# Kernel optimization log

Measured on AMD Instinct MI355X. Metric: run time of the kernel, lower is better.

The kernel has to match this reference:

```python
import jax, jax.numpy as jnp
import numpy as np

N = 4096
NEG_SLOPE = 0.2


def _gat_layer(x, src, dst, W, Wb, a, ab):
    # h = Linear(x); e_ij = a([h_i, h_j]) for each edge; dense softmax over dim=1; ELU
    h = x @ W + Wb                               # [N, D]
    D = h.shape[-1]
    e = h[src] @ a[:D] + h[dst] @ a[D:] + ab     # [E] per-edge attention logits
    n = x.shape[0]
    attn = jnp.full((n, n), -jnp.inf, dtype=x.dtype).at[src, dst].set(e)
    attn = jnp.where(attn > 0, attn, NEG_SLOPE * attn)   # leaky_relu (keeps -inf)
    attn = jax.nn.softmax(attn, axis=1)
    return jax.nn.elu(attn @ h)                  # sigma = ELU


def _multihead(x, src, dst, hW, hWb, ha, hab, oW, oWb, oa, oab):
    # concat=False: mean over head outputs, then out GATLayer
    heads = jax.vmap(lambda W, Wb, a, ab: _gat_layer(x, src, dst, W, Wb, a, ab))(hW, hWb, ha, hab)
    xm = heads.mean(axis=0)
    return _gat_layer(xm, src, dst, oW, oWb, oa, oab)


def setup_inputs() -> dict:
    key = jax.random.key(0)
    ks = jax.random.split(key, 20)
    in_dim, hid, out_dim, H, E = 512, 256, 128, 4, 131072
    x = jax.random.normal(ks[0], (N, in_dim), jnp.float32)
    edge_index = jax.random.randint(ks[1], (2, E), 0, N)
    # force self loops so every softmax row has at least one finite entry
    edge_index = edge_index.at[:, :N].set(jnp.broadcast_to(jnp.arange(N), (2, N)))

    def lin(k, shape, fan_in):
        return jax.random.uniform(k, shape, jnp.float32, -1.0, 1.0) / np.sqrt(fan_in).astype(np.float32)

    return {
        "x": x,
        "edge_index": edge_index,
        # layer 0 (MultiHeadGAT in_dim->hid)
        "l0_hW": lin(ks[2], (H, in_dim, hid), in_dim),
        "l0_hWb": lin(ks[3], (H, hid), in_dim),
        "l0_ha": lin(ks[4], (H, 2 * hid), 2 * hid),
        "l0_hab": lin(ks[5], (H,), 2 * hid),
        "l0_oW": lin(ks[6], (hid, hid), hid),
        "l0_oWb": lin(ks[7], (hid,), hid),
        "l0_oa": lin(ks[8], (2 * hid,), 2 * hid),
        "l0_oab": lin(ks[9], (), 2 * hid),
        # layer 1 (MultiHeadGAT hid->hid)
        "l1_hW": lin(ks[10], (H, hid, hid), hid),
        "l1_hWb": lin(ks[11], (H, hid), hid),
        "l1_ha": lin(ks[12], (H, 2 * hid), 2 * hid),
        "l1_hab": lin(ks[13], (H,), 2 * hid),
        "l1_oW": lin(ks[14], (hid, hid), hid),
        "l1_oWb": lin(ks[15], (hid,), hid),
        "l1_oa": lin(ks[16], (2 * hid,), 2 * hid),
        "l1_oab": lin(ks[17], (), 2 * hid),
        # final Linear(hid -> out_dim)
        "lin_W": lin(ks[18], (hid, out_dim), hid),
        "lin_b": lin(ks[19], (out_dim,), hid),
    }


def reference(x, edge_index, l0_hW, l0_hWb, l0_ha, l0_hab, l0_oW, l0_oWb, l0_oa, l0_oab,
              l1_hW, l1_hWb, l1_ha, l1_hab, l1_oW, l1_oWb, l1_oa, l1_oab, lin_W, lin_b):
    src, dst = edge_index[0], edge_index[1]
    lrelu = lambda v: jnp.where(v > 0, v, NEG_SLOPE * v)
    h = lrelu(_multihead(x, src, dst, l0_hW, l0_hWb, l0_ha, l0_hab, l0_oW, l0_oWb, l0_oa, l0_oab))
    h = lrelu(_multihead(h, src, dst, l1_hW, l1_hWb, l1_ha, l1_hab, l1_oW, l1_oWb, l1_oa, l1_oab))
    return h @ lin_W + lin_b  # [N, out_dim], flatten(1) is a no-op for 2D
```

## Files before the change

### kernel.cpp

```cpp
#include <hip/hip_runtime.h>
#include <hip/hip_bf16.h>
#include <math.h>

#define NEG_SLOPE 0.2f

constexpr int D = 256;
constexpr int HEADS = 4;
constexpr int MAXDEG = 2048;

typedef __attribute__((ext_vector_type(8))) short short8;
typedef __attribute__((ext_vector_type(4))) float floatx4;

__device__ inline unsigned short bf16_hi_trunc(float v) {
  return (unsigned short)(__float_as_uint(v) >> 16);
}
__device__ inline float bf16_tof(unsigned short u) {
  return __uint_as_float(((unsigned int)u) << 16);
}
__device__ inline unsigned short bf16_rn(float v) {
  unsigned int b = __float_as_uint(v);
  b += 0x7fffu + ((b >> 16) & 1u);
  return (unsigned short)(b >> 16);
}
__device__ inline void split2(float v, unsigned short& hi, unsigned short& lo) {
  hi = bf16_hi_trunc(v);
  lo = bf16_rn(v - bf16_tof(hi));
}

__global__ void zero_ints(int* __restrict__ p, int n) {
  int i = blockIdx.x * blockDim.x + threadIdx.x;
  if (i < n) p[i] = 0;
}

__global__ void count_kernel(const int* __restrict__ src, int* __restrict__ cnt, int E) {
  int k = blockIdx.x * blockDim.x + threadIdx.x;
  if (k < E) atomicAdd(&cnt[src[k]], 1);
}

__global__ __launch_bounds__(256) void scan_kernel(const int* __restrict__ cnt,
                                                   int* __restrict__ row_ptr, int Nn) {
  __shared__ int part[256];
  int tid = threadIdx.x;
  int per = Nn >> 8;
  int base = tid * per;
  int local[32];
  int s = 0;
  for (int j = 0; j < per; ++j) { local[j] = cnt[base + j]; s += local[j]; }
  part[tid] = s;
  __syncthreads();
  for (int off = 1; off < 256; off <<= 1) {
    int v = (tid >= off) ? part[tid - off] : 0;
    __syncthreads();
    part[tid] += v;
    __syncthreads();
  }
  int run = part[tid] - s;
  for (int j = 0; j < per; ++j) { row_ptr[base + j] = run; run += local[j]; }
  if (tid == 255) row_ptr[Nn] = run;
}

__global__ void fill_kernel(const int* __restrict__ src, const int* __restrict__ dst,
                            const int* __restrict__ row_ptr, int* __restrict__ cursor,
                            int* __restrict__ col, int E) {
  int k = blockIdx.x * blockDim.x + threadIdx.x;
  if (k < E) {
    int s = src[k];
    int pos = atomicAdd(&cursor[s], 1);
    col[row_ptr[s] + pos] = dst[k];
  }
}

__global__ __launch_bounds__(256) void dedupe_kernel(const int* __restrict__ row_ptr,
                                                     int* __restrict__ col, int Nn) {
  __shared__ int cs[MAXDEG];
  int i = blockIdx.x;
  int start = row_ptr[i];
  int len = row_ptr[i + 1] - start;
  if (len > MAXDEG) len = MAXDEG;
  int tid = threadIdx.x;
  for (int t = tid; t < len; t += 256) cs[t] = col[start + t];
  __syncthreads();
  for (int t = tid; t < len; t += 256) {
    int c = cs[t];
    bool dup = false;
    for (int s2 = 0; s2 < t; ++s2)
      if (cs[s2] == c) { dup = true; break; }
    if (dup) col[start + t] = -1;
  }
}

__global__ void split_kernel(const float* __restrict__ in, unsigned short* __restrict__ hi,
                             unsigned short* __restrict__ lo, int n4) {
  int idx = blockIdx.x * blockDim.x + threadIdx.x;
  if (idx < n4) {
    float4 v = ((const float4*)in)[idx];
    ushort4 h, l;
    split2(v.x, h.x, l.x);
    split2(v.y, h.y, l.y);
    split2(v.z, h.z, l.z);
    split2(v.w, h.w, l.w);
    ((ushort4*)hi)[idx] = h;
    ((ushort4*)lo)[idx] = l;
  }
}

__global__ __launch_bounds__(256) void transpose_split_kernel(
    const float* __restrict__ B, unsigned short* __restrict__ Thi,
    unsigned short* __restrict__ Tlo, int K, int N) {
  __shared__ float tile[32][33];
  const int t = threadIdx.x;
  const int k0 = blockIdx.x * 32, n0 = blockIdx.y * 32, h = blockIdx.z;
  const float* Bh = B + (size_t)h * K * N;
  const int tr = t >> 5, tc = t & 31;
#pragma unroll
  for (int i = 0; i < 4; ++i)
    tile[tr + 8 * i][tc] = Bh[(size_t)(k0 + tr + 8 * i) * N + (n0 + tc)];
  __syncthreads();
  unsigned short* ThiH = Thi + (size_t)h * N * K;
  unsigned short* TloH = Tlo + (size_t)h * N * K;
#pragma unroll
  for (int i = 0; i < 4; ++i) {
    int n = n0 + tr + 8 * i, k = k0 + tc;
    float v = tile[tc][tr + 8 * i];
    unsigned short hi, lo;
    split2(v, hi, lo);
    ThiH[(size_t)n * K + k] = hi;
    TloH[(size_t)n * K + k] = lo;
  }
}

__global__ __launch_bounds__(256) void transpose_split7_kernel(
    const float* __restrict__ l1hW, const float* __restrict__ B0,
    const float* __restrict__ B1, const float* __restrict__ B2,
    unsigned short* __restrict__ l1Thi, unsigned short* __restrict__ l1Tlo,
    unsigned short* __restrict__ T0h, unsigned short* __restrict__ T0l,
    unsigned short* __restrict__ T1h, unsigned short* __restrict__ T1l,
    unsigned short* __restrict__ T2h, unsigned short* __restrict__ T2l) {
  const int z = blockIdx.z;
  const int N = (z == 6) ? 128 : 256;
  const int K = 256;
  const int k0 = blockIdx.x * 32, n0 = blockIdx.y * 32;
  if (n0 >= N) return;
  const float* B;
  unsigned short *Thi, *Tlo;
  if (z < 4) {
    B = l1hW + (size_t)z * K * 256;
    Thi = l1Thi + (size_t)z * 256 * K;
    Tlo = l1Tlo + (size_t)z * 256 * K;
  } else if (z == 4) { B = B0; Thi = T0h; Tlo = T0l; }
  else if (z == 5)   { B = B1; Thi = T1h; Tlo = T1l; }
  else               { B = B2; Thi = T2h; Tlo = T2l; }
  __shared__ float tile[32][33];
  const int t = threadIdx.x;
  const int tr = t >> 5, tc = t & 31;
#pragma unroll
  for (int i = 0; i < 4; ++i)
    tile[tr + 8 * i][tc] = B[(size_t)(k0 + tr + 8 * i) * N + (n0 + tc)];
  __syncthreads();
#pragma unroll
  for (int i = 0; i < 4; ++i) {
    int n = n0 + tr + 8 * i, k = k0 + tc;
    float v = tile[tc][tr + 8 * i];
    unsigned short hi, lo;
    split2(v, hi, lo);
    Thi[(size_t)n * K + k] = hi;
    Tlo[(size_t)n * K + k] = lo;
  }
}

__global__ __launch_bounds__(256) void gemm_mfma_split(
    const unsigned short* __restrict__ Ahi, const unsigned short* __restrict__ Alo,
    const unsigned short* __restrict__ Bthi, const unsigned short* __restrict__ Btlo,
    const float* __restrict__ bias, float* __restrict__ C, unsigned short* __restrict__ Cb,
    const float* __restrict__ aptr, float* __restrict__ alphaB, float* __restrict__ betaB,
    int M, int N, int K) {
  constexpr int LSTR = 72;
  __shared__ unsigned short sA[2][64 * LSTR];
  __shared__ unsigned short sB[2][64 * LSTR];
  const int tid = threadIdx.x;
  const int bm = blockIdx.x * 64;
  const int gn = blockIdx.y * 64;
  const int head = (gn) / N;
  const int bn = gn - head * N;

  const int lane = tid & 63;
  const int wv = tid >> 6;
  const int wm = (wv & 1) * 32;
  const int wn = (wv >> 1) * 32;
  const int q = lane >> 4;
  const int l15 = lane & 15;

  floatx4 acc[2][2];
#pragma unroll
  for (int i = 0; i < 2; ++i)
#pragma unroll
    for (int j = 0; j < 2; ++j) acc[i][j] = (floatx4)0.0f;

  for (int k0 = 0; k0 < K; k0 += 64) {
    short8 ra[2][2], rb[2][2];
#pragma unroll
    for (int i = 0; i < 2; ++i) {
      const int c = tid + 256 * i;
      const int row = c >> 3, koff = (c & 7) << 3;
      const size_t aoff = (size_t)(bm + row) * K + k0 + koff;
      const size_t boff = (size_t)(gn + row) * K + k0 + koff;
      ra[0][i] = *(const short8*)(Ahi + aoff);
      ra[1][i] = *(const short8*)(Alo + aoff);
      rb[0][i] = *(const short8*)(Bthi + boff);
      rb[1][i] = *(const short8*)(Btlo + boff);
    }
    __syncthreads();
#pragma unroll
    for (int i = 0; i < 2; ++i) {
      const int c = tid + 256 * i;
      const int row = c >> 3, koff = (c & 7) << 3;
      *(short8*)(&sA[0][row * LSTR + koff]) = ra[0][i];
      *(short8*)(&sA[1][row * LSTR + koff]) = ra[1][i];
      *(short8*)(&sB[0][row * LSTR + koff]) = rb[0][i];
      *(short8*)(&sB[1][row * LSTR + koff]) = rb[1][i];
    }
    __syncthreads();
#pragma unroll
    for (int kc = 0; kc < 2; ++kc) {
      const int ko = kc * 32 + q * 8;
      short8 aH[2], aL[2], bH[2], bL[2];
#pragma unroll
      for (int i = 0; i < 2; ++i) {
        aH[i] = *(const short8*)(&sA[0][(wm + i * 16 + l15) * LSTR + ko]);
        aL[i] = *(const short8*)(&sA[1][(wm + i * 16 + l15) * LSTR + ko]);
        bH[i] = *(const short8*)(&sB[0][(wn + i * 16 + l15) * LSTR + ko]);
        bL[i] = *(const short8*)(&sB[1][(wn + i * 16 + l15) * LSTR + ko]);
      }
#pragma unroll
      for (int i = 0; i < 2; ++i)
#pragma unroll
        for (int j = 0; j < 2; ++j) {
          acc[i][j] = __builtin_amdgcn_mfma_f32_16x16x32_bf16(aH[i], bH[j], acc[i][j], 0, 0, 0);
          acc[i][j] = __builtin_amdgcn_mfma_f32_16x16x32_bf16(aH[i], bL[j], acc[i][j], 0, 0, 0);
          acc[i][j] = __builtin_amdgcn_mfma_f32_16x16x32_bf16(aL[i], bH[j], acc[i][j], 0, 0, 0);
        }
    }
  }
  const size_t cBase = (size_t)head * M * N;
  const int colh0 = bn + wn + l15;
  const int colh1 = colh0 + 16;
  const float bv0 = bias[head * N + colh0];
  const float bv1 = bias[head * N + colh1];
  float as0 = 0.f, as1 = 0.f, ad0 = 0.f, ad1 = 0.f;
  if (aptr) {
    as0 = aptr[head * 2 * N + colh0];
    as1 = aptr[head * 2 * N + colh1];
    ad0 = aptr[head * 2 * N + N + colh0];
    ad1 = aptr[head * 2 * N + N + colh1];
  }
#pragma unroll
  for (int i = 0; i < 2; ++i) {
    const int rowb = bm + wm + i * 16 + q * 4;
#pragma unroll
    for (int r = 0; r < 4; ++r) {
      const float o0 = acc[i][0][r] + bv0;
      const float o1 = acc[i][1][r] + bv1;
      if (Cb) {
        Cb[cBase + (size_t)(rowb + r) * N + colh0] = bf16_rn(o0);
        Cb[cBase + (size_t)(rowb + r) * N + colh1] = bf16_rn(o1);
      } else {
        C[cBase + (size_t)(rowb + r) * N + colh0] = o0;
        C[cBase + (size_t)(rowb + r) * N + colh1] = o1;
      }
      if (aptr) {
        float pa = o0 * as0 + o1 * as1;
        float pb = o0 * ad0 + o1 * ad1;
#pragma unroll
        for (int off = 1; off < 16; off <<= 1) {
          pa += __shfl_xor(pa, off, 64);
          pb += __shfl_xor(pb, off, 64);
        }
        if (l15 == 0) {
          atomicAdd(&alphaB[head * M + rowb + r], pa);
          atomicAdd(&betaB[head * M + rowb + r], pb);
        }
      }
    }
  }
}

__global__ __launch_bounds__(256) void gemm_bias(
    const float* __restrict__ A, const float* __restrict__ B,
    const float* __restrict__ bias, float* __restrict__ C,
    int M, int N, int K) {
  __shared__ float As[16][68];
  __shared__ float Bs[16][68];
  const int tid = threadIdx.x;
  const int bm = blockIdx.x * 64;
  const int gn = blockIdx.y * 64;
  const int head = gn / N;
  const int bn = gn - head * N;
  const float* Bh = B + (size_t)head * K * N;

  const int tx = tid & 15;
  const int ty = tid >> 4;
  const int am = tid >> 2;
  const int ak = (tid & 3) << 2;
  const int bk = tid >> 4;
  const int bn4 = (tid & 15) << 2;

  float acc[4][4] = {};

  for (int k0 = 0; k0 < K; k0 += 16) {
    float4 av = *(const float4*)(A + (size_t)(bm + am) * K + (k0 + ak));
    float4 bv = *(const float4*)(Bh + (size_t)(k0 + bk) * N + (bn + bn4));
    __syncthreads();
    As[ak + 0][am] = av.x;
    As[ak + 1][am] = av.y;
    As[ak + 2][am] = av.z;
    As[ak + 3][am] = av.w;
    *(float4*)(&Bs[bk][bn4]) = bv;
    __syncthreads();
#pragma unroll
    for (int k = 0; k < 16; ++k) {
      float4 aa = *(const float4*)(&As[k][ty << 2]);
      float4 bb = *(const float4*)(&Bs[k][tx << 2]);
      acc[0][0] += aa.x * bb.x; acc[0][1] += aa.x * bb.y; acc[0][2] += aa.x * bb.z; acc[0][3] += aa.x * bb.w;
      acc[1][0] += aa.y * bb.x; acc[1][1] += aa.y * bb.y; acc[1][2] += aa.y * bb.z; acc[1][3] += aa.y * bb.w;
      acc[2][0] += aa.z * bb.x; acc[2][1] += aa.z * bb.y; acc[2][2] += aa.z * bb.z; acc[2][3] += aa.z * bb.w;
      acc[3][0] += aa.w * bb.x; acc[3][1] += aa.w * bb.y; acc[3][2] += aa.w * bb.z; acc[3][3] += aa.w * bb.w;
    }
  }
  float* Ch = C + (size_t)head * M * N;
  const float* bh = bias + (size_t)head * N;
  const int ccol = bn + (tx << 2);
  float4 bias4 = *(const float4*)(bh + ccol);
#pragma unroll
  for (int r = 0; r < 4; ++r) {
    int row = bm + (ty << 2) + r;
    float4 o;
    o.x = acc[r][0] + bias4.x;
    o.y = acc[r][1] + bias4.y;
    o.z = acc[r][2] + bias4.z;
    o.w = acc[r][3] + bias4.w;
    *(float4*)(Ch + (size_t)row * N + ccol) = o;
  }
}

__global__ __launch_bounds__(256) void alphabeta_kernel(
    const float* __restrict__ h, const float* __restrict__ a,
    float* __restrict__ alpha, float* __restrict__ beta, int Nn) {
  __shared__ float reda[4], redb[4];
  const int i = blockIdx.x;
  const int hh = blockIdx.y;
  const int tid = threadIdx.x;
  const int lane = tid & 63, wid = tid >> 6;
  float v = h[((size_t)hh * Nn + i) * D + tid];
  float pa = v * a[hh * 2 * D + tid];
  float pb = v * a[hh * 2 * D + D + tid];
#pragma unroll
  for (int off = 32; off > 0; off >>= 1) {
    pa += __shfl_xor(pa, off, 64);
    pb += __shfl_xor(pb, off, 64);
  }
  if (lane == 0) { reda[wid] = pa; redb[wid] = pb; }
  __syncthreads();
  if (tid == 0) {
    alpha[hh * Nn + i] = reda[0] + reda[1] + reda[2] + reda[3];
    beta[hh * Nn + i] = redb[0] + redb[1] + redb[2] + redb[3];
  }
}

template <int BF16H>
__global__ __launch_bounds__(256) void attn2(
    const float* __restrict__ h, const unsigned short* __restrict__ hB,
    const float* __restrict__ alpha, const float* __restrict__ beta,
    const float* __restrict__ ab, const int* __restrict__ row_ptr,
    const int* __restrict__ col, float* __restrict__ out,
    unsigned short* __restrict__ oHi, unsigned short* __restrict__ oLo,
    int Nn, int H, int mode) {
  const int tid = threadIdx.x;
  const int lane = tid & 63;
  const int wv = tid >> 6;
  const int bx = blockIdx.x;
  const int head = bx % H;
  const int rowblk = bx / H;
  const int i = rowblk * 4 + wv;

  const float* hL = BF16H ? nullptr : (h + (size_t)head * Nn * D + (lane << 2));
  const unsigned short* hLB = BF16H ? (hB + (size_t)head * Nn * D + (lane << 2)) : nullptr;
  const float* betaH = beta + (size_t)head * Nn;
  const float ai = alpha[head * Nn + i] + ab[head];
  const int start = row_ptr[i];
  const int len = row_ptr[i + 1] - start;

  float m = -3.0e38f, s = 0.0f;
  float4 acc0 = make_float4(0.0f, 0.0f, 0.0f, 0.0f);
  float4 acc1 = make_float4(0.0f, 0.0f, 0.0f, 0.0f);

  for (int t0 = 0; t0 < len; t0 += 64) {
    const int t = t0 + lane;
    const int c = (t < len) ? col[start + t] : -1;
    float e = -3.0e38f;
    if (c >= 0) {
      e = ai + betaH[c];
      e = e > 0.0f ? e : NEG_SLOPE * e;
    }
    float cm = e;
#pragma unroll
    for (int off = 32; off > 0; off >>= 1) cm = fmaxf(cm, __shfl_xor(cm, off, 64));
    const float newm = fmaxf(m, cm);
    const float scale = __expf(m - newm);
    const float w = (c >= 0) ? __expf(e - newm) : 0.0f;
    float cs = w;
#pragma unroll
    for (int off = 32; off > 0; off >>= 1) cs += __shfl_xor(cs, off, 64);
    s = s * scale + cs;
    acc0.x *= scale; acc0.y *= scale; acc0.z *= scale; acc0.w *= scale;
    acc1.x *= scale; acc1.y *= scale; acc1.z *= scale; acc1.w *= scale;
    m = newm;

    const int cS = (c >= 0) ? c : 0;
    const int cnt = min(64, len - t0);
    int j = 0;
    if constexpr (BF16H) {
      for (; j + 4 <= cnt; j += 4) {
        const int c0 = __shfl(cS, j);     const float w0 = __shfl(w, j);
        const int c1 = __shfl(cS, j + 1); const float w1 = __shfl(w, j + 1);
        const int c2 = __shfl(cS, j + 2); const float w2 = __shfl(w, j + 2);
        const int c3 = __shfl(cS, j + 3); const float w3 = __shfl(w, j + 3);
        const ushort4 u0 = *(const ushort4*)(hLB + (size_t)c0 * D);
        const ushort4 u1 = *(const ushort4*)(hLB + (size_t)c1 * D);
        const ushort4 u2 = *(const ushort4*)(hLB + (size_t)c2 * D);
        const ushort4 u3 = *(const ushort4*)(hLB + (size_t)c3 * D);
        acc0.x += w0 * bf16_tof(u0.x); acc0.y += w0 * bf16_tof(u0.y);
        acc0.z += w0 * bf16_tof(u0.z); acc0.w += w0 * bf16_tof(u0.w);
        acc1.x += w1 * bf16_tof(u1.x); acc1.y += w1 * bf16_tof(u1.y);
        acc1.z += w1 * bf16_tof(u1.z); acc1.w += w1 * bf16_tof(u1.w);
        acc0.x += w2 * bf16_tof(u2.x); acc0.y += w2 * bf16_tof(u2.y);
        acc0.z += w2 * bf16_tof(u2.z); acc0.w += w2 * bf16_tof(u2.w);
        acc1.x += w3 * bf16_tof(u3.x); acc1.y += w3 * bf16_tof(u3.y);
        acc1.z += w3 * bf16_tof(u3.z); acc1.w += w3 * bf16_tof(u3.w);
      }
      for (; j < cnt; ++j) {
        const int cj = __shfl(cS, j);
        const float wj = __shfl(w, j);
        const ushort4 u = *(const ushort4*)(hLB + (size_t)cj * D);
        acc0.x += wj * bf16_tof(u.x); acc0.y += wj * bf16_tof(u.y);
        acc0.z += wj * bf16_tof(u.z); acc0.w += wj * bf16_tof(u.w);
      }
    } else {
      for (; j + 4 <= cnt; j += 4) {
        const int c0 = __shfl(cS, j);     const float w0 = __shfl(w, j);
        const int c1 = __shfl(cS, j + 1); const float w1 = __shfl(w, j + 1);
        const int c2 = __shfl(cS, j + 2); const float w2 = __shfl(w, j + 2);
        const int c3 = __shfl(cS, j + 3); const float w3 = __shfl(w, j + 3);
        const float4 h0 = *(const float4*)(hL + (size_t)c0 * D);
        const float4 h1 = *(const float4*)(hL + (size_t)c1 * D);
        const float4 h2 = *(const float4*)(hL + (size_t)c2 * D);
        const float4 h3 = *(const float4*)(hL + (size_t)c3 * D);
        acc0.x += w0 * h0.x; acc0.y += w0 * h0.y; acc0.z += w0 * h0.z; acc0.w += w0 * h0.w;
        acc1.x += w1 * h1.x; acc1.y += w1 * h1.y; acc1.z += w1 * h1.z; acc1.w += w1 * h1.w;
        acc0.x += w2 * h2.x; acc0.y += w2 * h2.y; acc0.z += w2 * h2.z; acc0.w += w2 * h2.w;
        acc1.x += w3 * h3.x; acc1.y += w3 * h3.y; acc1.z += w3 * h3.z; acc1.w += w3 * h3.w;
      }
      for (; j < cnt; ++j) {
        const int cj = __shfl(cS, j);
        const float wj = __shfl(w, j);
        const float4 hv = *(const float4*)(hL + (size_t)cj * D);
        acc0.x += wj * hv.x; acc0.y += wj * hv.y;
        acc0.z += wj * hv.z; acc0.w += wj * hv.w;
      }
    }
  }

  const float inv = 1.0f / s;
  float4 v;
  v.x = (acc0.x + acc1.x) * inv; v.y = (acc0.y + acc1.y) * inv;
  v.z = (acc0.z + acc1.z) * inv; v.w = (acc0.w + acc1.w) * inv;
  v.x = v.x > 0.0f ? v.x : expm1f(v.x);
  v.y = v.y > 0.0f ? v.y : expm1f(v.y);
  v.z = v.z > 0.0f ? v.z : expm1f(v.z);
  v.w = v.w > 0.0f ? v.w : expm1f(v.w);

  if (mode == 1 || mode == 3) {
    v.x = v.x > 0.0f ? v.x : NEG_SLOPE * v.x;
    v.y = v.y > 0.0f ? v.y : NEG_SLOPE * v.y;
    v.z = v.z > 0.0f ? v.z : NEG_SLOPE * v.z;
    v.w = v.w > 0.0f ? v.w : NEG_SLOPE * v.w;
    if (mode == 1) {
      *(float4*)(out + (size_t)i * D + (lane << 2)) = v;
    } else {
      ushort4 h4, l4;
      split2(v.x, h4.x, l4.x);
      split2(v.y, h4.y, l4.y);
      split2(v.z, h4.z, l4.z);
      split2(v.w, h4.w, l4.w);
      const size_t q4 = ((size_t)i * D >> 2) + lane;
      ((ushort4*)oHi)[q4] = h4;
      ((ushort4*)oLo)[q4] = l4;
    }
  } else if (mode == 0) {
    *(float4*)(out + ((size_t)head * Nn + i) * D + (lane << 2)) = v;
  } else {
    const float invH = 1.0f / (float)H;
    float* o = out + (size_t)i * D + (lane << 2);
    atomicAdd(o + 0, invH * v.x);
    atomicAdd(o + 1, invH * v.y);
    atomicAdd(o + 2, invH * v.z);
    atomicAdd(o + 3, invH * v.w);
  }
}

__global__ __launch_bounds__(256) void mean4_kernel(
    float* __restrict__ hsep, unsigned short* __restrict__ outHi,
    unsigned short* __restrict__ outLo, int total4, int mode) {
  int idx = blockIdx.x * blockDim.x + threadIdx.x;
  if (idx < total4) {
    float4* p = (float4*)hsep;
    float4 a = p[idx], b = p[idx + total4], c = p[idx + 2 * total4], d = p[idx + 3 * total4];
    float4 o;
    o.x = 0.25f * (a.x + b.x + c.x + d.x);
    o.y = 0.25f * (a.y + b.y + c.y + d.y);
    o.z = 0.25f * (a.z + b.z + c.z + d.z);
    o.w = 0.25f * (a.w + b.w + c.w + d.w);
    if (mode == 0) {
      p[idx] = o;
    } else {
      ushort4 h4, l4;
      split2(o.x, h4.x, l4.x);
      split2(o.y, h4.y, l4.y);
      split2(o.z, h4.z, l4.z);
      split2(o.w, h4.w, l4.w);
      ((ushort4*)outHi)[idx] = h4;
      ((ushort4*)outLo)[idx] = l4;
    }
  }
}

__global__ void zero_floats(float* __restrict__ p, int n) {
  int i = blockIdx.x * blockDim.x + threadIdx.x;
  if (i < n) p[i] = 0.0f;
}

extern "C" void kernel_launch(void* const* d_in, const int* in_sizes, int n_in,
                              void* d_out, int out_size, void* d_ws, size_t ws_size,
                              hipStream_t stream) {
  const float* x = (const float*)d_in[0];
  const int* eidx = (const int*)d_in[1];
  const float* l0_hW = (const float*)d_in[2];
  const float* l0_hWb = (const float*)d_in[3];
  const float* l0_ha = (const float*)d_in[4];
  const float* l0_hab = (const float*)d_in[5];
  const float* l0_oW = (const float*)d_in[6];
  const float* l0_oWb = (const float*)d_in[7];
  const float* l0_oa = (const float*)d_in[8];
  const float* l0_oab = (const float*)d_in[9];
  const float* l1_hW = (const float*)d_in[10];
  const float* l1_hWb = (const float*)d_in[11];
  const float* l1_ha = (const float*)d_in[12];
  const float* l1_hab = (const float*)d_in[13];
  const float* l1_oW = (const float*)d_in[14];
  const float* l1_oWb = (const float*)d_in[15];
  const float* l1_oa = (const float*)d_in[16];
  const float* l1_oab = (const float*)d_in[17];
  const float* lin_W = (const float*)d_in[18];
  const float* lin_b = (const float*)d_in[19];

  const int in_dim = 512;
  const int Nn = in_sizes[0] / in_dim;
  const int E = in_sizes[1] / 2;
  const int out_dim = 128;

  char* wsp = (char*)d_ws;
  auto alloc = [&](size_t bytes) {
    char* p = wsp;
    wsp += (bytes + 255) & ~(size_t)255;
    return p;
  };
  const size_t ndBytes = sizeof(float) * (size_t)Nn * D;
  const size_t mfmaNeed = 52000000;
  const bool mfma = ws_size >= mfmaNeed;

  if (mfma) {
    unsigned short* hbufB = (unsigned short*)alloc((size_t)HEADS * Nn * D * 2);
    unsigned short* houtB = (unsigned short*)alloc((size_t)Nn * D * 2);
    float* hsep   = (float*)alloc(ndBytes * HEADS);
    unsigned short* xhi  = (unsigned short*)alloc((size_t)Nn * in_dim * 2);
    unsigned short* xlo  = (unsigned short*)alloc((size_t)Nn * in_dim * 2);
    unsigned short* x1hi = xhi;
    unsigned short* x1lo = xlo;
    unsigned short* xmhi = (unsigned short*)alloc((size_t)Nn * D * 2);
    unsigned short* xmlo = (unsigned short*)alloc((size_t)Nn * D * 2);
    unsigned short* l0hHi = (unsigned short*)alloc((size_t)HEADS * in_dim * D * 2);
    unsigned short* l0hLo = (unsigned short*)alloc((size_t)HEADS * in_dim * D * 2);
    unsigned short* l1hHi = (unsigned short*)alloc((size_t)HEADS * D * D * 2);
    unsigned short* l1hLo = (unsigned short*)alloc((size_t)HEADS * D * D * 2);
    unsigned short* l0oHi = (unsigned short*)alloc((size_t)D * D * 2);
    unsigned short* l0oLo = (unsigned short*)alloc((size_t)D * D * 2);
    unsigned short* l1oHi = (unsigned short*)alloc((size_t)D * D * 2);
    unsigned short* l1oLo = (unsigned short*)alloc((size_t)D * D * 2);
    unsigned short* linHi = (unsigned short*)alloc((size_t)D * out_dim * 2);
    unsigned short* linLo = (unsigned short*)alloc((size_t)D * out_dim * 2);
    int* cnt     = (int*)alloc(sizeof(int) * Nn);
    int* cursor  = (int*)alloc(sizeof(int) * Nn);
    float* abz   = (float*)alloc(sizeof(float) * 4 * 2 * HEADS * (size_t)Nn);
    int* row_ptr = (int*)alloc(sizeof(int) * (Nn + 1));
    int* col     = (int*)alloc(sizeof(int) * E);
    auto alphaS = [&](int s) { return abz + (size_t)s * 2 * HEADS * Nn; };
    auto betaS  = [&](int s) { return abz + (size_t)s * 2 * HEADS * Nn + HEADS * Nn; };

    const int* src = eidx;
    const int* dst = eidx + E;

    const int zeroN = 2 * Nn + 4 * 2 * HEADS * Nn;
    zero_ints<<<(zeroN + 255) / 256, 256, 0, stream>>>(cnt, zeroN);
    count_kernel<<<(E + 255) / 256, 256, 0, stream>>>(src, cnt, E);
    scan_kernel<<<1, 256, 0, stream>>>(cnt, row_ptr, Nn);
    fill_kernel<<<(E + 255) / 256, 256, 0, stream>>>(src, dst, row_ptr, cursor, col, E);
    dedupe_kernel<<<Nn, 256, 0, stream>>>(row_ptr, col, Nn);

    split_kernel<<<(Nn * in_dim / 4 + 255) / 256, 256, 0, stream>>>(x, xhi, xlo, Nn * in_dim / 4);
    transpose_split_kernel<<<dim3(in_dim / 32, D / 32, HEADS), 256, 0, stream>>>(l0_hW, l0hHi, l0hLo, in_dim, D);
    transpose_split7_kernel<<<dim3(8, 8, 7), 256, 0, stream>>>(
        l1_hW, l0_oW, l1_oW, lin_W, l1hHi, l1hLo, l0oHi, l0oLo, l1oHi, l1oLo, linHi, linLo);

    const int total4 = Nn * D / 4;
    const int meanBlocks = (total4 + 255) / 256;

    gemm_mfma_split<<<dim3(Nn / 64, HEADS * D / 64), 256, 0, stream>>>(
        xhi, xlo, l0hHi, l0hLo, l0_hWb, nullptr, hbufB, l0_ha, alphaS(0), betaS(0), Nn, D, in_dim);
    attn2<1><<<HEADS * (Nn / 4), 256, 0, stream>>>(nullptr, hbufB, alphaS(0), betaS(0), l0_hab,
                                                   row_ptr, col, hsep, nullptr, nullptr, Nn, HEADS, 0);
    mean4_kernel<<<meanBlocks, 256, 0, stream>>>(hsep, xmhi, xmlo, total4, 1);
    gemm_mfma_split<<<dim3(Nn / 64, D / 64), 256, 0, stream>>>(
        xmhi, xmlo, l0oHi, l0oLo, l0_oWb, nullptr, houtB, l0_oa, alphaS(1), betaS(1), Nn, D, D);
    attn2<1><<<Nn / 4, 256, 0, stream>>>(nullptr, houtB, alphaS(1), betaS(1), l0_oab,
                                         row_ptr, col, nullptr, x1hi, x1lo, Nn, 1, 3);

    gemm_mfma_split<<<dim3(Nn / 64, HEADS * D / 64), 256, 0, stream>>>(
        x1hi, x1lo, l1hHi, l1hLo, l1_hWb, nullptr, hbufB, l1_ha, alphaS(2), betaS(2), Nn, D, D);
    attn2<1><<<HEADS * (Nn / 4), 256, 0, stream>>>(nullptr, hbufB, alphaS(2), betaS(2), l1_hab,
                                                   row_ptr, col, hsep, nullptr, nullptr, Nn, HEADS, 0);
    mean4_kernel<<<meanBlocks, 256, 0, stream>>>(hsep, xmhi, xmlo, total4, 1);
    gemm_mfma_split<<<dim3(Nn / 64, D / 64), 256, 0, stream>>>(
        xmhi, xmlo, l1oHi, l1oLo, l1_oWb, nullptr, houtB, l1_oa, alphaS(3), betaS(3), Nn, D, D);
    attn2<1><<<Nn / 4, 256, 0, stream>>>(nullptr, houtB, alphaS(3), betaS(3), l1_oab,
                                         row_ptr, col, nullptr, x1hi, x1lo, Nn, 1, 3);

    gemm_mfma_split<<<dim3(Nn / 64, out_dim / 64), 256, 0, stream>>>(
        x1hi, x1lo, linHi, linLo, lin_b, (float*)d_out, nullptr, nullptr, nullptr, nullptr, Nn, out_dim, D);
    return;
  }

  const size_t smallBytes = sizeof(float) * 2 * HEADS * (size_t)Nn + sizeof(int) * (3 * Nn + 1 + E) + 4096;
  const bool staged = ws_size >= (8 * ndBytes + 2 * ndBytes + smallBytes + 65536);

  float* hbuf  = (float*)alloc(ndBytes * HEADS);
  float* hsep  = staged ? (float*)alloc(ndBytes * HEADS) : nullptr;
  float* xm    = staged ? hsep : (float*)alloc(ndBytes);
  float* x1    = (float*)alloc(ndBytes);
  float* hout  = (float*)alloc(ndBytes);
  float* alpha = (float*)alloc(sizeof(float) * HEADS * (size_t)Nn);
  float* beta  = (float*)alloc(sizeof(float) * HEADS * (size_t)Nn);
  int* cnt     = (int*)alloc(sizeof(int) * Nn);
  int* cursor  = (int*)alloc(sizeof(int) * Nn);
  int* row_ptr = (int*)alloc(sizeof(int) * (Nn + 1));
  int* col     = (int*)alloc(sizeof(int) * E);

  const int* src = eidx;
  const int* dst = eidx + E;

  zero_ints<<<(2 * Nn + 255) / 256, 256, 0, stream>>>(cnt, 2 * Nn);
  count_kernel<<<(E + 255) / 256, 256, 0, stream>>>(src, cnt, E);
  scan_kernel<<<1, 256, 0, stream>>>(cnt, row_ptr, Nn);
  fill_kernel<<<(E + 255) / 256, 256, 0, stream>>>(src, dst, row_ptr, cursor, col, E);
  dedupe_kernel<<<Nn, 256, 0, stream>>>(row_ptr, col, Nn);

  const int total4 = Nn * D / 4;
  const int meanBlocks = (total4 + 255) / 256;

  gemm_bias<<<dim3(Nn / 64, HEADS * D / 64), 256, 0, stream>>>(x, l0_hW, l0_hWb, hbuf, Nn, D, in_dim);
  alphabeta_kernel<<<dim3(Nn, HEADS), 256, 0, stream>>>(hbuf, l0_ha, alpha, beta, Nn);
  if (staged) {
    attn2<0><<<HEADS * (Nn / 4), 256, 0, stream>>>(hbuf, nullptr, alpha, beta, l0_hab, row_ptr, col, hsep, nullptr, nullptr, Nn, HEADS, 0);
    mean4_kernel<<<meanBlocks, 256, 0, stream>>>(hsep, nullptr, nullptr, total4, 0);
  } else {
    zero_floats<<<(Nn * D + 255) / 256, 256, 0, stream>>>(xm, Nn * D);
    attn2<0><<<HEADS * (Nn / 4), 256, 0, stream>>>(hbuf, nullptr, alpha, beta, l0_hab, row_ptr, col, xm, nullptr, nullptr, Nn, HEADS, 2);
  }
  gemm_bias<<<dim3(Nn / 64, D / 64), 256, 0, stream>>>(xm, l0_oW, l0_oWb, hout, Nn, D, D);
  alphabeta_kernel<<<dim3(Nn, 1), 256, 0, stream>>>(hout, l0_oa, alpha, beta, Nn);
  attn2<0><<<Nn / 4, 256, 0, stream>>>(hout, nullptr, alpha, beta, l0_oab, row_ptr, col, x1, nullptr, nullptr, Nn, 1, 1);

  gemm_bias<<<dim3(Nn / 64, HEADS * D / 64), 256, 0, stream>>>(x1, l1_hW, l1_hWb, hbuf, Nn, D, D);
  alphabeta_kernel<<<dim3(Nn, HEADS), 256, 0, stream>>>(hbuf, l1_ha, alpha, beta, Nn);
  if (staged) {
    attn2<0><<<HEADS * (Nn / 4), 256, 0, stream>>>(hbuf, nullptr, alpha, beta, l1_hab, row_ptr, col, hsep, nullptr, nullptr, Nn, HEADS, 0);
    mean4_kernel<<<meanBlocks, 256, 0, stream>>>(hsep, nullptr, nullptr, total4, 0);
  } else {
    zero_floats<<<(Nn * D + 255) / 256, 256, 0, stream>>>(xm, Nn * D);
    attn2<0><<<HEADS * (Nn / 4), 256, 0, stream>>>(hbuf, nullptr, alpha, beta, l1_hab, row_ptr, col, xm, nullptr, nullptr, Nn, HEADS, 2);
  }
  gemm_bias<<<dim3(Nn / 64, D / 64), 256, 0, stream>>>(xm, l1_oW, l1_oWb, hout, Nn, D, D);
  alphabeta_kernel<<<dim3(Nn, 1), 256, 0, stream>>>(hout, l1_oa, alpha, beta, Nn);
  attn2<0><<<Nn / 4, 256, 0, stream>>>(hout, nullptr, alpha, beta, l1_oab, row_ptr, col, x1, nullptr, nullptr, Nn, 1, 1);

  gemm_bias<<<dim3(Nn / 64, out_dim / 64), 256, 0, stream>>>(x1, lin_W, lin_b, (float*)d_out, Nn, out_dim, D);
}
```

Baseline: 276.2 us.

## Fold head-mean into out-projection GEMM and merge prep kernels

The per-head attention outputs are now written directly as split bf16 hi/lo in a [N, H*D] layout. The out-layer weight is replicated four times, scaled by 0.25, so the out-projection GEMM with K=H*D performs the head mean itself, which removes the fp32 hsep buffer and the mean4 kernels. The x split and all weight transpose-splits are merged into one prep launch. The cost is a 4x larger K in the out-projection GEMMs and a change in rounding, since each head is split separately before the mean.

```diff
diff --git a/kernel.cpp b/kernel.cpp
--- a/kernel.cpp
+++ b/kernel.cpp
@@ -89,82 +89,97 @@
   }
 }
 
-__global__ void split_kernel(const float* __restrict__ in, unsigned short* __restrict__ hi,
-                             unsigned short* __restrict__ lo, int n4) {
-  int idx = blockIdx.x * blockDim.x + threadIdx.x;
-  if (idx < n4) {
-    float4 v = ((const float4*)in)[idx];
-    ushort4 h, l;
-    split2(v.x, h.x, l.x);
-    split2(v.y, h.y, l.y);
-    split2(v.z, h.z, l.z);
-    split2(v.w, h.w, l.w);
-    ((ushort4*)hi)[idx] = h;
-    ((ushort4*)lo)[idx] = l;
-  }
-}
-
-__global__ __launch_bounds__(256) void transpose_split_kernel(
-    const float* __restrict__ B, unsigned short* __restrict__ Thi,
-    unsigned short* __restrict__ Tlo, int K, int N) {
+__global__ __launch_bounds__(256) void prep_kernel(
+    const float* __restrict__ x, unsigned short* __restrict__ xhi, unsigned short* __restrict__ xlo,
+    int xN4,
+    const float* __restrict__ l0hW, unsigned short* __restrict__ l0hHi, unsigned short* __restrict__ l0hLo,
+    const float* __restrict__ l1hW, unsigned short* __restrict__ l1hHi, unsigned short* __restrict__ l1hLo,
+    const float* __restrict__ l0oW, unsigned short* __restrict__ l0oHi, unsigned short* __restrict__ l0oLo,
+    const float* __restrict__ l1oW, unsigned short* __restrict__ l1oHi, unsigned short* __restrict__ l1oLo,
+    const float* __restrict__ linW, unsigned short* __restrict__ linHi, unsigned short* __restrict__ linLo) {
+  const int b = blockIdx.x;
+  const int t = threadIdx.x;
+  if (b < 2048) {
+    int idx = b * 256 + t;
+    if (idx < xN4) {
+      float4 v = ((const float4*)x)[idx];
+      ushort4 h, l;
+      split2(v.x, h.x, l.x);
+      split2(v.y, h.y, l.y);
+      split2(v.z, h.z, l.z);
+      split2(v.w, h.w, l.w);
+      ((ushort4*)xhi)[idx] = h;
+      ((ushort4*)xlo)[idx] = l;
+    }
+    return;
+  }
   __shared__ float tile[32][33];
-  const int t = threadIdx.x;
-  const int k0 = blockIdx.x * 32, n0 = blockIdx.y * 32, h = blockIdx.z;
-  const float* Bh = B + (size_t)h * K * N;
   const int tr = t >> 5, tc = t & 31;
+  if (b < 2560) {
+    const int bi = b - 2048;
+    const int kb = bi & 15;
+    const int nb = (bi >> 4) & 7;
+    const int h = bi >> 7;
+    const int K = 512, N = 256;
+    const int k0 = kb * 32, n0 = nb * 32;
+    const float* B = l0hW + (size_t)h * K * N;
+#pragma unroll
+    for (int i = 0; i < 4; ++i)
+      tile[tr + 8 * i][tc] = B[(size_t)(k0 + tr + 8 * i) * N + (n0 + tc)];
+    __syncthreads();
+    unsigned short* Thi = l0hHi + (size_t)h * N * K;
+    unsigned short* Tlo = l0hLo + (size_t)h * N * K;
+#pragma unroll
+    for (int i = 0; i < 4; ++i) {
+      int n = n0 + tr + 8 * i, k = k0 + tc;
+      float v = tile[tc][tr + 8 * i];
+      unsigned short hi, lo;
+      split2(v, hi, lo);
+      Thi[(size_t)n * K + k] = hi;
+      Tlo[(size_t)n * K + k] = lo;
+    }
+    return;
+  }
+  const int bi = b - 2560;
+  const int kb = bi & 7;
+  const int nb = (bi >> 3) & 7;
+  const int z = bi >> 6;
+  const int K = 256;
+  const int N = (z == 6) ? 128 : 256;
+  const int k0 = kb * 32, n0 = nb * 32;
+  if (n0 >= N) return;
+  const float* B;
+  unsigned short *Thi, *Tlo;
+  bool repl4 = false;
+  if (z < 4) {
+    B = l1hW + (size_t)z * K * 256;
+    Thi = l1hHi + (size_t)z * 256 * K;
+    Tlo = l1hLo + (size_t)z * 256 * K;
+  } else if (z == 4) { B = l0oW; Thi = l0oHi; Tlo = l0oLo; repl4 = true; }
+  else if (z == 5)   { B = l1oW; Thi = l1oHi; Tlo = l1oLo; repl4 = true; }
+  else               { B = linW; Thi = linHi; Tlo = linLo; }
 #pragma unroll
   for (int i = 0; i < 4; ++i)
-    tile[tr + 8 * i][tc] = Bh[(size_t)(k0 + tr + 8 * i) * N + (n0 + tc)];
+    tile[tr + 8 * i][tc] = B[(size_t)(k0 + tr + 8 * i) * N + (n0 + tc)];
   __syncthreads();
-  unsigned short* ThiH = Thi + (size_t)h * N * K;
-  unsigned short* TloH = Tlo + (size_t)h * N * K;
 #pragma unroll
   for (int i = 0; i < 4; ++i) {
     int n = n0 + tr + 8 * i, k = k0 + tc;
     float v = tile[tc][tr + 8 * i];
-    unsigned short hi, lo;
-    split2(v, hi, lo);
-    ThiH[(size_t)n * K + k] = hi;
-    TloH[(size_t)n * K + k] = lo;
-  }
-}
-
-__global__ __launch_bounds__(256) void transpose_split7_kernel(
-    const float* __restrict__ l1hW, const float* __restrict__ B0,
-    const float* __restrict__ B1, const float* __restrict__ B2,
-    unsigned short* __restrict__ l1Thi, unsigned short* __restrict__ l1Tlo,
-    unsigned short* __restrict__ T0h, unsigned short* __restrict__ T0l,
-    unsigned short* __restrict__ T1h, unsigned short* __restrict__ T1l,
-    unsigned short* __restrict__ T2h, unsigned short* __restrict__ T2l) {
-  const int z = blockIdx.z;
-  const int N = (z == 6) ? 128 : 256;
-  const int K = 256;
-  const int k0 = blockIdx.x * 32, n0 = blockIdx.y * 32;
-  if (n0 >= N) return;
-  const float* B;
-  unsigned short *Thi, *Tlo;
-  if (z < 4) {
-    B = l1hW + (size_t)z * K * 256;
-    Thi = l1Thi + (size_t)z * 256 * K;
-    Tlo = l1Tlo + (size_t)z * 256 * K;
-  } else if (z == 4) { B = B0; Thi = T0h; Tlo = T0l; }
-  else if (z == 5)   { B = B1; Thi = T1h; Tlo = T1l; }
-  else               { B = B2; Thi = T2h; Tlo = T2l; }
-  __shared__ float tile[32][33];
-  const int t = threadIdx.x;
-  const int tr = t >> 5, tc = t & 31;
-#pragma unroll
-  for (int i = 0; i < 4; ++i)
-    tile[tr + 8 * i][tc] = B[(size_t)(k0 + tr + 8 * i) * N + (n0 + tc)];
-  __syncthreads();
-#pragma unroll
-  for (int i = 0; i < 4; ++i) {
-    int n = n0 + tr + 8 * i, k = k0 + tc;
-    float v = tile[tc][tr + 8 * i];
-    unsigned short hi, lo;
-    split2(v, hi, lo);
-    Thi[(size_t)n * K + k] = hi;
-    Tlo[(size_t)n * K + k] = lo;
+    if (repl4) {
+      unsigned short hi, lo;
+      split2(0.25f * v, hi, lo);
+#pragma unroll
+      for (int h = 0; h < 4; ++h) {
+        Thi[(size_t)n * 1024 + h * 256 + k] = hi;
+        Tlo[(size_t)n * 1024 + h * 256 + k] = lo;
+      }
+    } else {
+      unsigned short hi, lo;
+      split2(v, hi, lo);
+      Thi[(size_t)n * K + k] = hi;
+      Tlo[(size_t)n * K + k] = lo;
+    }
   }
 }
 
@@ -496,7 +511,18 @@
       ((ushort4*)oLo)[q4] = l4;
     }
   } else if (mode == 0) {
-    *(float4*)(out + ((size_t)head * Nn + i) * D + (lane << 2)) = v;
+    if constexpr (BF16H) {
+      ushort4 h4, l4;
+      split2(v.x, h4.x, l4.x);
+      split2(v.y, h4.y, l4.y);
+      split2(v.z, h4.z, l4.z);
+      split2(v.w, h4.w, l4.w);
+      const size_t q4 = ((size_t)i * H + head) * (D / 4) + lane;
+      ((ushort4*)oHi)[q4] = h4;
+      ((ushort4*)oLo)[q4] = l4;
+    } else {
+      *(float4*)(out + ((size_t)head * Nn + i) * D + (lane << 2)) = v;
+    }
   } else {
     const float invH = 1.0f / (float)H;
     float* o = out + (size_t)i * D + (lane << 2);
@@ -580,21 +606,20 @@
   if (mfma) {
     unsigned short* hbufB = (unsigned short*)alloc((size_t)HEADS * Nn * D * 2);
     unsigned short* houtB = (unsigned short*)alloc((size_t)Nn * D * 2);
-    float* hsep   = (float*)alloc(ndBytes * HEADS);
+    unsigned short* aHi   = (unsigned short*)alloc((size_t)Nn * HEADS * D * 2);
+    unsigned short* aLo   = (unsigned short*)alloc((size_t)Nn * HEADS * D * 2);
     unsigned short* xhi  = (unsigned short*)alloc((size_t)Nn * in_dim * 2);
     unsigned short* xlo  = (unsigned short*)alloc((size_t)Nn * in_dim * 2);
     unsigned short* x1hi = xhi;
     unsigned short* x1lo = xlo;
-    unsigned short* xmhi = (unsigned short*)alloc((size_t)Nn * D * 2);
-    unsigned short* xmlo = (unsigned short*)alloc((size_t)Nn * D * 2);
     unsigned short* l0hHi = (unsigned short*)alloc((size_t)HEADS * in_dim * D * 2);
     unsigned short* l0hLo = (unsigned short*)alloc((size_t)HEADS * in_dim * D * 2);
     unsigned short* l1hHi = (unsigned short*)alloc((size_t)HEADS * D * D * 2);
     unsigned short* l1hLo = (unsigned short*)alloc((size_t)HEADS * D * D * 2);
-    unsigned short* l0oHi = (unsigned short*)alloc((size_t)D * D * 2);
-    unsigned short* l0oLo = (unsigned short*)alloc((size_t)D * D * 2);
-    unsigned short* l1oHi = (unsigned short*)alloc((size_t)D * D * 2);
-    unsigned short* l1oLo = (unsigned short*)alloc((size_t)D * D * 2);
+    unsigned short* l0oHi = (unsigned short*)alloc((size_t)D * 4 * D * 2);
+    unsigned short* l0oLo = (unsigned short*)alloc((size_t)D * 4 * D * 2);
+    unsigned short* l1oHi = (unsigned short*)alloc((size_t)D * 4 * D * 2);
+    unsigned short* l1oLo = (unsigned short*)alloc((size_t)D * 4 * D * 2);
     unsigned short* linHi = (unsigned short*)alloc((size_t)D * out_dim * 2);
     unsigned short* linLo = (unsigned short*)alloc((size_t)D * out_dim * 2);
     int* cnt     = (int*)alloc(sizeof(int) * Nn);
@@ -615,31 +640,26 @@
     fill_kernel<<<(E + 255) / 256, 256, 0, stream>>>(src, dst, row_ptr, cursor, col, E);
     dedupe_kernel<<<Nn, 256, 0, stream>>>(row_ptr, col, Nn);
 
-    split_kernel<<<(Nn * in_dim / 4 + 255) / 256, 256, 0, stream>>>(x, xhi, xlo, Nn * in_dim / 4);
-    transpose_split_kernel<<<dim3(in_dim / 32, D / 32, HEADS), 256, 0, stream>>>(l0_hW, l0hHi, l0hLo, in_dim, D);
-    transpose_split7_kernel<<<dim3(8, 8, 7), 256, 0, stream>>>(
-        l1_hW, l0_oW, l1_oW, lin_W, l1hHi, l1hLo, l0oHi, l0oLo, l1oHi, l1oLo, linHi, linLo);
-
-    const int total4 = Nn * D / 4;
-    const int meanBlocks = (total4 + 255) / 256;
+    prep_kernel<<<3008, 256, 0, stream>>>(
+        x, xhi, xlo, Nn * in_dim / 4,
+        l0_hW, l0hHi, l0hLo, l1_hW, l1hHi, l1hLo,
+        l0_oW, l0oHi, l0oLo, l1_oW, l1oHi, l1oLo, lin_W, linHi, linLo);
 
     gemm_mfma_split<<<dim3(Nn / 64, HEADS * D / 64), 256, 0, stream>>>(
         xhi, xlo, l0hHi, l0hLo, l0_hWb, nullptr, hbufB, l0_ha, alphaS(0), betaS(0), Nn, D, in_dim);
     attn2<1><<<HEADS * (Nn / 4), 256, 0, stream>>>(nullptr, hbufB, alphaS(0), betaS(0), l0_hab,
-                                                   row_ptr, col, hsep, nullptr, nullptr, Nn, HEADS, 0);
-    mean4_kernel<<<meanBlocks, 256, 0, stream>>>(hsep, xmhi, xmlo, total4, 1);
+                                                   row_ptr, col, nullptr, aHi, aLo, Nn, HEADS, 0);
     gemm_mfma_split<<<dim3(Nn / 64, D / 64), 256, 0, stream>>>(
-        xmhi, xmlo, l0oHi, l0oLo, l0_oWb, nullptr, houtB, l0_oa, alphaS(1), betaS(1), Nn, D, D);
+        aHi, aLo, l0oHi, l0oLo, l0_oWb, nullptr, houtB, l0_oa, alphaS(1), betaS(1), Nn, D, HEADS * D);
     attn2<1><<<Nn / 4, 256, 0, stream>>>(nullptr, houtB, alphaS(1), betaS(1), l0_oab,
                                          row_ptr, col, nullptr, x1hi, x1lo, Nn, 1, 3);
 
     gemm_mfma_split<<<dim3(Nn / 64, HEADS * D / 64), 256, 0, stream>>>(
         x1hi, x1lo, l1hHi, l1hLo, l1_hWb, nullptr, hbufB, l1_ha, alphaS(2), betaS(2), Nn, D, D);
     attn2<1><<<HEADS * (Nn / 4), 256, 0, stream>>>(nullptr, hbufB, alphaS(2), betaS(2), l1_hab,
-                                                   row_ptr, col, hsep, nullptr, nullptr, Nn, HEADS, 0);
-    mean4_kernel<<<meanBlocks, 256, 0, stream>>>(hsep, xmhi, xmlo, total4, 1);
+                                                   row_ptr, col, nullptr, aHi, aLo, Nn, HEADS, 0);
     gemm_mfma_split<<<dim3(Nn / 64, D / 64), 256, 0, stream>>>(
-        xmhi, xmlo, l1oHi, l1oLo, l1_oWb, nullptr, houtB, l1_oa, alphaS(3), betaS(3), Nn, D, D);
+        aHi, aLo, l1oHi, l1oLo, l1_oWb, nullptr, houtB, l1_oa, alphaS(3), betaS(3), Nn, D, HEADS * D);
     attn2<1><<<Nn / 4, 256, 0, stream>>>(nullptr, houtB, alphaS(3), betaS(3), l1_oab,
                                          row_ptr, col, nullptr, x1hi, x1lo, Nn, 1, 3);
 
```

After: 288.6 us. 4.5% more time.
